# Optimization experiments

Hardware: AMD Instinct MI355X
Metric: run time of the kernel (lower is better)

The kernel has to match this reference:

```python
import jax, jax.numpy as jnp
import numpy as np

KNN_K = 16
EPS = 1e-5


def _knn_idx(p, k):
    # p: [B,3,N] -> idx [B,N,k] of nearest neighbors (self excluded)
    pt = jnp.swapaxes(p, 1, 2)                      # [B,N,3]
    xx = jnp.sum(pt * pt, axis=-1)                  # [B,N]
    inner = jnp.einsum('bnd,bmd->bnm', pt, pt)      # [B,N,N]
    dist = -(xx[:, :, None] - 2.0 * inner + xx[:, None, :])  # -||pi-pj||^2
    N = pt.shape[1]
    dist = dist - 1e9 * jnp.eye(N, dtype=dist.dtype)
    return jax.lax.top_k(dist, k)[1]


def _ln(x, g, b):
    mu = jnp.mean(x, axis=-1, keepdims=True)
    var = jnp.mean((x - mu) ** 2, axis=-1, keepdims=True)
    return (x - mu) * jax.lax.rsqrt(var + EPS) * g + b


_gather = jax.vmap(lambda a, i: a[i])  # a:[N,C], i:[N,k] -> [N,k,C]


def setup_inputs() -> dict:
    key = jax.random.key(0)
    ks = jax.random.split(key, 24)
    Cin, C, B, N = 64, 128, 8, 2048
    s = lambda k_, shp, fan: jax.random.normal(k_, shp, jnp.float32) * (1.0 / np.sqrt(fan))
    return {
        'x': jax.random.normal(ks[0], (B, Cin, N), jnp.float32),
        'p': jax.random.normal(ks[1], (B, 3, N), jnp.float32),
        'Win': s(ks[2], (C, Cin), Cin), 'bin_': jnp.zeros((C,), jnp.float32),
        'Wq': s(ks[3], (C, C), C), 'Wk': s(ks[4], (C, C), C), 'Wv': s(ks[5], (C, C), C),
        'Wd1': s(ks[6], (C, 3), 3), 'bd1': jnp.zeros((C,), jnp.float32),
        'Wd2': s(ks[7], (C, C), C), 'bd2': jnp.zeros((C,), jnp.float32),
        'Wa': s(ks[8], (C, C), C), 'ba': jnp.zeros((C,), jnp.float32),
        'g1': jnp.ones((C,), jnp.float32), 'b1': jnp.zeros((C,), jnp.float32),
        'g2': jnp.ones((C,), jnp.float32), 'b2': jnp.zeros((C,), jnp.float32),
        'Wf1': s(ks[9], (4 * C, C), C), 'bf1': jnp.zeros((4 * C,), jnp.float32),
        'Wf2': s(ks[10], (C, 4 * C), 4 * C), 'bf2': jnp.zeros((C,), jnp.float32),
    }


def reference(x, p, Win, bin_, Wq, Wk, Wv, Wd1, bd1, Wd2, bd2, Wa, ba,
              g1, b1, g2, b2, Wf1, bf1, Wf2, bf2) -> jnp.ndarray:
    B, _, N = x.shape
    k = min(KNN_K, max(1, N - 1))
    # in_proj (conv1x1 == per-point linear); work in [B,N,C]
    h = jnp.einsum('oc,bcn->bno', Win, x) + bin_          # [B,N,C]
    hn = _ln(h, g1, b1)
    idx = _knn_idx(p, k)                                  # [B,N,k] (int)
    q = hn @ Wq.T                                         # [B,N,C]
    k_all = hn @ Wk.T
    v_all = hn @ Wv.T
    k_j = _gather(k_all, idx)                             # [B,N,k,C]
    v_j = _gather(v_all, idx)
    pt = jnp.swapaxes(p, 1, 2)                            # [B,N,3]
    p_j = _gather(pt, idx)                                # [B,N,k,3]
    rel = pt[:, :, None, :] - p_j                         # [B,N,k,3]
    d = jax.nn.relu(rel @ Wd1.T + bd1) @ Wd2.T + bd2      # [B,N,k,C]
    logits = (q[:, :, None, :] - k_j + d) @ Wa.T + ba     # [B,N,k,C]
    a = jax.nn.softmax(logits, axis=2)                    # softmax over neighbors
    y = jnp.sum(a * (v_j + d), axis=2)                    # [B,N,C]
    h = h + y
    h2 = _ln(h, g2, b2)
    h = h + jax.nn.relu(h2 @ Wf1.T + bf1) @ Wf2.T + bf2
    return jnp.swapaxes(h, 1, 2)                          # [B,C,N]
```

## Files before the change

### kernel.cpp

```cpp
#include <hip/hip_runtime.h>

typedef __bf16 bf16_t;
typedef __bf16 bf16x8 __attribute__((ext_vector_type(8)));
typedef __bf16 bf16x2 __attribute__((ext_vector_type(2)));
typedef float  f32x4  __attribute__((ext_vector_type(4)));

#define MFMA16(a,b,c) __builtin_amdgcn_mfma_f32_16x16x32_bf16((a),(b),(c),0,0,0)

#define BB 8
#define NN 2048
#define CC 128
#define CIN 64
#define KNB 16
#define BNT (BB*NN)

static __device__ __forceinline__ int remap256(int x) { return ((x & 7) << 5) | (x >> 3); }

static __device__ __forceinline__ bf16x8 cvt8(const float* src) {
  f32x4 a0 = *(const f32x4*)src;
  f32x4 a1 = *(const f32x4*)(src + 4);
  bf16x8 fr;
  fr[0] = (__bf16)a0[0]; fr[1] = (__bf16)a0[1]; fr[2] = (__bf16)a0[2]; fr[3] = (__bf16)a0[3];
  fr[4] = (__bf16)a1[0]; fr[5] = (__bf16)a1[1]; fr[6] = (__bf16)a1[2]; fr[7] = (__bf16)a1[3];
  return fr;
}

__global__ __launch_bounds__(256) void compw_k(
    const float* __restrict__ Wq, const float* __restrict__ Wk, const float* __restrict__ Wv,
    const float* __restrict__ Wd2, const float* __restrict__ Wa,
    const float* __restrict__ Wf1, const float* __restrict__ Wf2,
    bf16_t* __restrict__ Wqb, bf16_t* __restrict__ Wkb, bf16_t* __restrict__ Wvb,
    bf16_t* __restrict__ Wd2b, bf16_t* __restrict__ Wab,
    bf16_t* __restrict__ Wf1b, bf16_t* __restrict__ Wf2b) {
  int mat = blockIdx.y;
  int nel = (mat >= 5) ? 65536 : 16384;
  const float* S = mat == 0 ? Wq : mat == 1 ? Wk : mat == 2 ? Wv : mat == 3 ? Wd2
                 : mat == 4 ? Wa : mat == 5 ? Wf1 : Wf2;
  bf16_t* D = mat == 0 ? Wqb : mat == 1 ? Wkb : mat == 2 ? Wvb : mat == 3 ? Wd2b
            : mat == 4 ? Wab : mat == 5 ? Wf1b : Wf2b;
  for (int i = blockIdx.x * 256 + threadIdx.x; i * 8 < nel; i += 2048)
    *(bf16x8*)(D + i * 8) = cvt8(S + i * 8);
}

__global__ __launch_bounds__(256) void inproj_ln_k(
    const float* __restrict__ x, const float* __restrict__ Win, const float* __restrict__ bin,
    const float* __restrict__ g1, const float* __restrict__ b1,
    float* __restrict__ h, bf16_t* __restrict__ hnb) {
  __shared__ bf16_t As[64 * 72];
  __shared__ bf16_t Bs[128 * 72];
  __shared__ float hs[64 * 132];
  int t = threadIdx.x;
  int lane = t & 63, w = t >> 6, quad = lane >> 4, l15 = lane & 15;
  int mBase = remap256(blockIdx.x) * 64;
  int b = mBase >> 11, n0 = mBase & (NN - 1);
  const float* xb = x + (size_t)b * CIN * NN;
  {
    int k = t >> 2, part = t & 3;
    #pragma unroll
    for (int i = 0; i < 4; ++i) {
      f32x4 v = *(const f32x4*)(xb + (size_t)k * NN + n0 + part * 16 + i * 4);
      #pragma unroll
      for (int j2 = 0; j2 < 4; ++j2) As[(part * 16 + i * 4 + j2) * 72 + k] = (__bf16)v[j2];
    }
  }
  {
    int row = t >> 1, seg = (t & 1) * 32;
    #pragma unroll
    for (int i = 0; i < 4; ++i)
      *(bf16x8*)(&Bs[row * 72 + seg + i * 8]) = cvt8(Win + (size_t)row * CIN + seg + i * 8);
  }
  __syncthreads();
  f32x4 acc[2][4] = {};
  #pragma unroll
  for (int s = 0; s < 2; ++s) {
    bf16x8 af[4];
    #pragma unroll
    for (int mt = 0; mt < 4; ++mt)
      af[mt] = *(const bf16x8*)(&As[(mt * 16 + l15) * 72 + s * 32 + quad * 8]);
    #pragma unroll
    for (int t2 = 0; t2 < 2; ++t2) {
      bf16x8 bfr = *(const bf16x8*)(&Bs[((w * 2 + t2) * 16 + l15) * 72 + s * 32 + quad * 8]);
      #pragma unroll
      for (int mt = 0; mt < 4; ++mt) acc[t2][mt] = MFMA16(af[mt], bfr, acc[t2][mt]);
    }
  }
  #pragma unroll
  for (int t2 = 0; t2 < 2; ++t2) {
    int col = (w * 2 + t2) * 16 + l15;
    float bv = bin[col];
    #pragma unroll
    for (int mt = 0; mt < 4; ++mt)
      #pragma unroll
      for (int reg = 0; reg < 4; ++reg)
        hs[(mt * 16 + quad * 4 + reg) * 132 + col] = acc[t2][mt][reg] + bv;
  }
  __syncthreads();
  {
    int row = t >> 2, c0 = (t & 3) * 32;
    float v[32];
    #pragma unroll
    for (int i = 0; i < 8; ++i) *(f32x4*)(v + i * 4) = *(const f32x4*)(&hs[row * 132 + c0 + i * 4]);
    float s1 = 0.f, s2 = 0.f;
    #pragma unroll
    for (int i = 0; i < 32; ++i) { s1 += v[i]; s2 += v[i] * v[i]; }
    s1 += __shfl_xor(s1, 1); s1 += __shfl_xor(s1, 2);
    s2 += __shfl_xor(s2, 1); s2 += __shfl_xor(s2, 2);
    float mu = s1 * (1.f / CC);
    float var = s2 * (1.f / CC) - mu * mu;
    float rs = rsqrtf(var + 1e-5f);
    float* hrow = h + (size_t)(mBase + row) * CC + c0;
    #pragma unroll
    for (int i = 0; i < 8; ++i) *(f32x4*)(hrow + i * 4) = *(const f32x4*)(v + i * 4);
    bf16_t* hnrow = hnb + (size_t)(mBase + row) * CC + c0;
    #pragma unroll
    for (int i = 0; i < 4; ++i) {
      f32x4 g4a = ((const f32x4*)g1)[(c0 >> 2) + i * 2],     g4b = ((const f32x4*)g1)[(c0 >> 2) + i * 2 + 1];
      f32x4 b4a = ((const f32x4*)b1)[(c0 >> 2) + i * 2],     b4b = ((const f32x4*)b1)[(c0 >> 2) + i * 2 + 1];
      bf16x8 o;
      #pragma unroll
      for (int j = 0; j < 4; ++j) o[j]     = (__bf16)((v[i * 8 + j]     - mu) * rs * g4a[j] + b4a[j]);
      #pragma unroll
      for (int j = 0; j < 4; ++j) o[4 + j] = (__bf16)((v[i * 8 + 4 + j] - mu) * rs * g4b[j] + b4b[j]);
      *(bf16x8*)(hnrow + i * 8) = o;
    }
  }
}

static __device__ __forceinline__ void cas(double& a, double& b) {
  double lo = fmin(a, b), hi = fmax(a, b); a = lo; b = hi;
}
#define S8(K,o) \
  cas(K[o+0],K[o+1]); cas(K[o+2],K[o+3]); cas(K[o+4],K[o+5]); cas(K[o+6],K[o+7]); \
  cas(K[o+0],K[o+2]); cas(K[o+1],K[o+3]); cas(K[o+4],K[o+6]); cas(K[o+5],K[o+7]); \
  cas(K[o+1],K[o+2]); cas(K[o+5],K[o+6]); \
  cas(K[o+0],K[o+4]); cas(K[o+1],K[o+5]); cas(K[o+2],K[o+6]); cas(K[o+3],K[o+7]); \
  cas(K[o+2],K[o+4]); cas(K[o+3],K[o+5]); \
  cas(K[o+1],K[o+2]); cas(K[o+3],K[o+4]); cas(K[o+5],K[o+6]);
#define M8(K,a,b) \
  K[a+0]=fmin(K[a+0],K[b+7]); K[a+1]=fmin(K[a+1],K[b+6]); K[a+2]=fmin(K[a+2],K[b+5]); K[a+3]=fmin(K[a+3],K[b+4]); \
  K[a+4]=fmin(K[a+4],K[b+3]); K[a+5]=fmin(K[a+5],K[b+2]); K[a+6]=fmin(K[a+6],K[b+1]); K[a+7]=fmin(K[a+7],K[b+0]); \
  cas(K[a+0],K[a+4]); cas(K[a+1],K[a+5]); cas(K[a+2],K[a+6]); cas(K[a+3],K[a+7]); \
  cas(K[a+0],K[a+2]); cas(K[a+1],K[a+3]); cas(K[a+4],K[a+6]); cas(K[a+5],K[a+7]); \
  cas(K[a+0],K[a+1]); cas(K[a+2],K[a+3]); cas(K[a+4],K[a+5]); cas(K[a+6],K[a+7]);

static __device__ void knn_impl(float* sp, const float* __restrict__ p,
                                int* __restrict__ idxo, int bid) {
  float* px = sp; float* py = sp + NN; float* pz = sp + 2 * NN;
  int t = threadIdx.x;
  int b = bid >> 9;
  int g = bid & 511;
  const float* pb = p + (size_t)b * 3 * NN;
  for (int i = t; i < NN; i += 256) { px[i] = pb[i]; py[i] = pb[NN + i]; pz[i] = pb[2 * NN + i]; }
  __syncthreads();
  int w = t >> 6, lane = t & 63;
  int n = g * 4 + w;
  float pnx = px[n], pny = py[n], pnz = pz[n];
  double key[32];
  #pragma unroll
  for (int s = 0; s < 32; ++s) {
    int m = s * 64 + lane;
    float dx = pnx - px[m], dy = pny - py[m], dz = pnz - pz[m];
    float dist = dx * dx + dy * dy + dz * dz;
    unsigned db = (m == n) ? 0x7F800000u : __float_as_uint(dist);
    key[s] = __hiloint2double((int)db, m);
  }
  S8(key, 0); S8(key, 8); S8(key, 16); S8(key, 24);
  M8(key, 0, 8); M8(key, 16, 24); M8(key, 0, 16);
  const double DINF = __hiloint2double(0x7F900000, 0);
  int* myout = idxo + ((size_t)b * NN + n) * KNB;
  #pragma unroll 1
  for (int r = 0; r < 16; ++r) {
    double gm = key[0];
    #pragma unroll
    for (int off = 1; off < 64; off <<= 1) {
      double o = __shfl_xor(gm, off);
      gm = fmin(gm, o);
    }
    if (lane == 0) myout[r] = __double2loint(gm);
    bool win = (key[0] == gm);
    key[0] = win ? key[1] : key[0];
    key[1] = win ? key[2] : key[1];
    key[2] = win ? key[3] : key[2];
    key[3] = win ? key[4] : key[3];
    key[4] = win ? key[5] : key[4];
    key[5] = win ? key[6] : key[5];
    key[6] = win ? key[7] : key[6];
    key[7] = win ? DINF   : key[7];
  }
}

template<int EPI>
static __device__ void gemm_body(bf16_t* As, bf16_t* Bs,
    const bf16_t* __restrict__ Ab, const bf16_t* __restrict__ Wb, const float* __restrict__ bias,
    float* __restrict__ outF, bf16_t* __restrict__ outB, const float* __restrict__ resid,
    int mBase, int nBase, int Ncol, int Kdim) {
  int t = threadIdx.x;
  int lane = t & 63, w = t >> 6, quad = lane >> 4, l15 = lane & 15;
  int r = t >> 2, seg = (t & 3) * 8;
  f32x4 acc[4] = {{0,0,0,0},{0,0,0,0},{0,0,0,0},{0,0,0,0}};
  for (int k0 = 0; k0 < Kdim; k0 += 32) {
    __syncthreads();
    *(bf16x8*)(&As[r * 40 + seg]) = *(const bf16x8*)(Ab + (size_t)(mBase + r) * Kdim + k0 + seg);
    *(bf16x8*)(&Bs[r * 40 + seg]) = *(const bf16x8*)(Wb + (size_t)(nBase + r) * Kdim + k0 + seg);
    __syncthreads();
    bf16x8 bfr = *(const bf16x8*)(&Bs[(w * 16 + l15) * 40 + quad * 8]);
    #pragma unroll
    for (int mt = 0; mt < 4; ++mt) {
      bf16x8 afr = *(const bf16x8*)(&As[(mt * 16 + l15) * 40 + quad * 8]);
      acc[mt] = MFMA16(afr, bfr, acc[mt]);
    }
  }
  int n = nBase + w * 16 + l15;
  float bv = bias ? bias[n] : 0.f;
  #pragma unroll
  for (int mt = 0; mt < 4; ++mt) {
    #pragma unroll
    for (int reg = 0; reg < 4; ++reg) {
      int m = mBase + mt * 16 + quad * 4 + reg;
      float val = acc[mt][reg] + bv;
      if (EPI == 0) {
        outF[(size_t)m * Ncol + n] = val;
      } else if (EPI == 1) {
        outB[(size_t)m * Ncol + n] = (__bf16)fmaxf(val, 0.f);
      } else if (EPI == 3) {
        outB[(size_t)m * Ncol + n] = (__bf16)val;
      } else {
        val += resid[(size_t)m * CC + n];
        int bo = m >> 11, np = m & (NN - 1);
        outF[((size_t)bo * CC + n) * NN + np] = val;
      }
    }
  }
}

template<int EPI>
__global__ __launch_bounds__(256) void gemm_k(
    const bf16_t* __restrict__ Ab, const bf16_t* __restrict__ Wb, const float* __restrict__ bias,
    float* __restrict__ outF, bf16_t* __restrict__ outB, const float* __restrict__ resid,
    int Ncol, int Kdim) {
  __shared__ bf16_t As[64 * 40];
  __shared__ bf16_t Bs[64 * 40];
  gemm_body<EPI>(As, Bs, Ab, Wb, bias, outF, outB, resid,
                 remap256(blockIdx.x) * 64, blockIdx.y * 64, Ncol, Kdim);
}

__global__ __launch_bounds__(256) void knn_qkv_k(
    const float* __restrict__ p, int* __restrict__ idxo,
    const bf16_t* __restrict__ hnb,
    const bf16_t* __restrict__ Wqb, const bf16_t* __restrict__ Wkb, const bf16_t* __restrict__ Wvb,
    float* __restrict__ q, bf16_t* __restrict__ kb, bf16_t* __restrict__ vb) {
  __shared__ __align__(16) char smem[3 * NN * 4];
  if (blockIdx.x < 4096) {
    knn_impl((float*)smem, p, idxo, blockIdx.x);
  } else {
    bf16_t* As = (bf16_t*)smem;
    bf16_t* Bs = As + 64 * 40;
    int bx = blockIdx.x - 4096;
    int yy = bx >> 8, xx = bx & 255;
    int sel = yy >> 1;
    int mB = remap256(xx) * 64, nB = (yy & 1) * 64;
    if (sel == 0)      gemm_body<0>(As, Bs, hnb, Wqb, nullptr, q,  nullptr, nullptr, mB, nB, CC, CC);
    else if (sel == 1) gemm_body<3>(As, Bs, hnb, Wkb, nullptr, nullptr, kb, nullptr, mB, nB, CC, CC);
    else               gemm_body<3>(As, Bs, hnb, Wvb, nullptr, nullptr, vb, nullptr, mB, nB, CC, CC);
  }
}

__global__ __launch_bounds__(256, 3) void attn_k(
    const float* __restrict__ qbuf, const bf16_t* __restrict__ kbuf, const bf16_t* __restrict__ vbuf,
    const float* __restrict__ p, const int* __restrict__ idx,
    const float* __restrict__ Wd1, const float* __restrict__ bd1,
    const bf16_t* __restrict__ Wd2b, const float* __restrict__ bd2,
    const bf16_t* __restrict__ Wab, const float* __restrict__ ba,
    const float* __restrict__ g2, const float* __restrict__ b2,
    const float* __restrict__ h, float* __restrict__ hres, bf16_t* __restrict__ h2) {
  __shared__ bf16_t ts[64 * 136];
  __shared__ float hrs[4 * 128];
  __shared__ f32x4 wd1s[128];
  __shared__ f32x4 rels4[64];
  __shared__ int idxs[64];
  int t = threadIdx.x;
  int lane = t & 63, w = t >> 6, quad = lane >> 4, l15 = lane & 15;
  int batch = blockIdx.x & 7, grp = blockIdx.x >> 3;
  int bn0 = batch * NN + grp * 4;
  int b = batch;
  const float* pb = p + (size_t)b * 3 * NN;
  int col0 = w * 32 + l15;
  int col1 = col0 + 16;

  bf16x8 Bd[2][4];
  #pragma unroll
  for (int t2 = 0; t2 < 2; ++t2) {
    int row = w * 32 + t2 * 16 + l15;
    #pragma unroll
    for (int s = 0; s < 4; ++s)
      Bd[t2][s] = *(const bf16x8*)(Wd2b + (size_t)row * CC + s * 32 + quad * 8);
  }

  if (t < 64) {
    int jj = idx[(size_t)bn0 * KNB + t];
    idxs[t] = jj;
    int npt = grp * 4 + (t >> 4);
    f32x4 rv;
    rv[0] = pb[npt]          - pb[jj];
    rv[1] = pb[NN + npt]     - pb[NN + jj];
    rv[2] = pb[2 * NN + npt] - pb[2 * NN + jj];
    rv[3] = 0.f;
    rels4[t] = rv;
  }
  if (t < 128) {
    f32x4 wv;
    wv[0] = Wd1[t * 3]; wv[1] = Wd1[t * 3 + 1]; wv[2] = Wd1[t * 3 + 2]; wv[3] = bd1[t];
    wd1s[t] = wv;
  }
  __syncthreads();

  float qv[2][4];
  #pragma unroll
  for (int mt = 0; mt < 4; ++mt) {
    qv[0][mt] = qbuf[(size_t)(bn0 + mt) * CC + col0];
    qv[1][mt] = qbuf[(size_t)(bn0 + mt) * CC + col1];
  }
  float kreg[2][4][4];
  #pragma unroll
  for (int mt = 0; mt < 4; ++mt)
    #pragma unroll
    for (int reg = 0; reg < 4; ++reg) {
      size_t base = (size_t)(b * NN + idxs[mt * 16 + quad * 4 + reg]) * CC;
      kreg[0][mt][reg] = (float)kbuf[base + col0];
      kreg[1][mt][reg] = (float)kbuf[base + col1];
    }

  f32x4 relv[4];
  #pragma unroll
  for (int mt = 0; mt < 4; ++mt) relv[mt] = rels4[mt * 16 + l15];
  f32x4 accd[2][4] = {};
  #pragma unroll
  for (int s = 0; s < 4; ++s) {
    bf16x8 af[4];
    #pragma unroll
    for (int j = 0; j < 8; ++j) {
      f32x4 wv = wd1s[s * 32 + quad * 8 + j];
      #pragma unroll
      for (int mt = 0; mt < 4; ++mt) {
        float tv = fmaf(wv[0], relv[mt][0], fmaf(wv[1], relv[mt][1], fmaf(wv[2], relv[mt][2], wv[3])));
        af[mt][j] = (__bf16)fmaxf(tv, 0.f);
      }
    }
    #pragma unroll
    for (int t2 = 0; t2 < 2; ++t2)
      #pragma unroll
      for (int mt = 0; mt < 4; ++mt)
        accd[t2][mt] = MFMA16(af[mt], Bd[t2][s], accd[t2][mt]);
  }

  {
    float b2v0 = bd2[col0], b2v1 = bd2[col1];
    #pragma unroll
    for (int mt = 0; mt < 4; ++mt)
      #pragma unroll
      for (int reg = 0; reg < 4; ++reg) {
        int row = mt * 16 + quad * 4 + reg;
        float d0 = accd[0][mt][reg] + b2v0;
        float d1 = accd[1][mt][reg] + b2v1;
        accd[0][mt][reg] = d0;
        accd[1][mt][reg] = d1;
        ts[row * 136 + col0] = (__bf16)(qv[0][mt] - kreg[0][mt][reg] + d0);
        ts[row * 136 + col1] = (__bf16)(qv[1][mt] - kreg[1][mt][reg] + d1);
      }
  }
  __syncthreads();

  float vreg[2][4][4];
  #pragma unroll
  for (int mt = 0; mt < 4; ++mt)
    #pragma unroll
    for (int reg = 0; reg < 4; ++reg) {
      size_t base = (size_t)(b * NN + idxs[mt * 16 + quad * 4 + reg]) * CC;
      vreg[0][mt][reg] = (float)vbuf[base + col0];
      vreg[1][mt][reg] = (float)vbuf[base + col1];
    }
  float hv[2][4];
  if (quad == 0) {
    #pragma unroll
    for (int mt = 0; mt < 4; ++mt) {
      hv[0][mt] = h[(size_t)(bn0 + mt) * CC + col0];
      hv[1][mt] = h[(size_t)(bn0 + mt) * CC + col1];
    }
  }
  bf16x8 Ba[2][4];
  #pragma unroll
  for (int t2 = 0; t2 < 2; ++t2) {
    int row = w * 32 + t2 * 16 + l15;
    #pragma unroll
    for (int s = 0; s < 4; ++s)
      Ba[t2][s] = *(const bf16x8*)(Wab + (size_t)row * CC + s * 32 + quad * 8);
  }

  f32x4 accl[2][4] = {};
  #pragma unroll
  for (int s = 0; s < 4; ++s) {
    bf16x8 af[4];
    #pragma unroll
    for (int mt = 0; mt < 4; ++mt)
      af[mt] = *(const bf16x8*)(&ts[(mt * 16 + l15) * 136 + s * 32 + quad * 8]);
    #pragma unroll
    for (int t2 = 0; t2 < 2; ++t2)
      #pragma unroll
      for (int mt = 0; mt < 4; ++mt)
        accl[t2][mt] = MFMA16(af[mt], Ba[t2][s], accl[t2][mt]);
  }

  #pragma unroll
  for (int t2 = 0; t2 < 2; ++t2) {
    int col = t2 ? col1 : col0;
    float bav = ba[col];
    #pragma unroll
    for (int mt = 0; mt < 4; ++mt) {
      float lv0 = accl[t2][mt][0] + bav, lv1 = accl[t2][mt][1] + bav;
      float lv2 = accl[t2][mt][2] + bav, lv3 = accl[t2][mt][3] + bav;
      float mx = fmaxf(fmaxf(lv0, lv1), fmaxf(lv2, lv3));
      mx = fmaxf(mx, __shfl_xor(mx, 16));
      mx = fmaxf(mx, __shfl_xor(mx, 32));
      float e0 = __expf(lv0 - mx), e1 = __expf(lv1 - mx);
      float e2 = __expf(lv2 - mx), e3 = __expf(lv3 - mx);
      float ss = e0 + e1 + e2 + e3;
      ss += __shfl_xor(ss, 16); ss += __shfl_xor(ss, 32);
      float yv = e0 * (vreg[t2][mt][0] + accd[t2][mt][0])
               + e1 * (vreg[t2][mt][1] + accd[t2][mt][1])
               + e2 * (vreg[t2][mt][2] + accd[t2][mt][2])
               + e3 * (vreg[t2][mt][3] + accd[t2][mt][3]);
      yv += __shfl_xor(yv, 16); yv += __shfl_xor(yv, 32);
      if (quad == 0) {
        float hvv = hv[t2][mt] + yv / ss;
        hres[(size_t)(bn0 + mt) * CC + col] = hvv;
        hrs[mt * 128 + col] = hvv;
      }
    }
  }
  __syncthreads();

  {
    int c0 = lane * 2;
    float v0 = hrs[w * 128 + c0], v1 = hrs[w * 128 + c0 + 1];
    float s1 = v0 + v1, s2 = v0 * v0 + v1 * v1;
    #pragma unroll
    for (int off = 1; off < 64; off <<= 1) { s1 += __shfl_xor(s1, off); s2 += __shfl_xor(s2, off); }
    float mu = s1 * (1.f / CC);
    float var = s2 * (1.f / CC) - mu * mu;
    float rs = rsqrtf(var + 1e-5f);
    bf16x2 o;
    o[0] = (__bf16)((v0 - mu) * rs * g2[c0] + b2[c0]);
    o[1] = (__bf16)((v1 - mu) * rs * g2[c0 + 1] + b2[c0 + 1]);
    *(bf16x2*)(h2 + (size_t)(bn0 + w) * CC + c0) = o;
  }
}

extern "C" void kernel_launch(void* const* d_in, const int* in_sizes, int n_in,
                              void* d_out, int out_size, void* d_ws, size_t ws_size,
                              hipStream_t stream) {
  const float* x   = (const float*)d_in[0];
  const float* p   = (const float*)d_in[1];
  const float* Win = (const float*)d_in[2];
  const float* bin = (const float*)d_in[3];
  const float* Wq  = (const float*)d_in[4];
  const float* Wk  = (const float*)d_in[5];
  const float* Wv  = (const float*)d_in[6];
  const float* Wd1 = (const float*)d_in[7];
  const float* bd1 = (const float*)d_in[8];
  const float* Wd2 = (const float*)d_in[9];
  const float* bd2 = (const float*)d_in[10];
  const float* Wa  = (const float*)d_in[11];
  const float* ba  = (const float*)d_in[12];
  const float* g1  = (const float*)d_in[13];
  const float* b1  = (const float*)d_in[14];
  const float* g2  = (const float*)d_in[15];
  const float* b2  = (const float*)d_in[16];
  const float* Wf1 = (const float*)d_in[17];
  const float* bf1 = (const float*)d_in[18];
  const float* Wf2 = (const float*)d_in[19];
  const float* bf2 = (const float*)d_in[20];
  float* out = (float*)d_out;

  const size_t SZ = (size_t)BNT * CC;
  float* wsf = (float*)d_ws;
  float*  h    = wsf;
  bf16_t* hnb  = (bf16_t*)(wsf + SZ);
  float*  hres = wsf + SZ;
  float*  q    = wsf + 2 * SZ;
  bf16_t* kb   = (bf16_t*)(wsf + 3 * SZ);
  bf16_t* vb   = kb + SZ;
  bf16_t* g    = (bf16_t*)(wsf + 2 * SZ);
  bf16_t* h2   = (bf16_t*)(wsf + 4 * SZ);
  int*    idxw = (int*)(wsf + 4 * SZ + SZ / 2);
  bf16_t* Wqb  = (bf16_t*)(idxw + (size_t)BNT * KNB);
  bf16_t* Wkb  = Wqb  + 16384;
  bf16_t* Wvb  = Wkb  + 16384;
  bf16_t* Wd2b = Wvb  + 16384;
  bf16_t* Wab  = Wd2b + 16384;
  bf16_t* Wf1b = Wab  + 16384;
  bf16_t* Wf2b = Wf1b + 65536;

  compw_k<<<dim3(8, 7), 256, 0, stream>>>(Wq, Wk, Wv, Wd2, Wa, Wf1, Wf2,
                                          Wqb, Wkb, Wvb, Wd2b, Wab, Wf1b, Wf2b);
  inproj_ln_k<<<BNT / 64, 256, 0, stream>>>(x, Win, bin, g1, b1, h, hnb);
  knn_qkv_k<<<4096 + 1536, 256, 0, stream>>>(p, idxw, hnb, Wqb, Wkb, Wvb, q, kb, vb);
  attn_k<<<BNT / 4, 256, 0, stream>>>(q, kb, vb, p, idxw, Wd1, bd1, Wd2b, bd2, Wab, ba,
                                      g2, b2, h, hres, h2);
  gemm_k<1><<<dim3(BNT / 64, 8), 256, 0, stream>>>(h2, Wf1b, bf1, nullptr, g, nullptr, 4 * CC, CC);
  gemm_k<2><<<dim3(BNT / 64, 2), 256, 0, stream>>>(g, Wf2b, bf2, out, nullptr, hres, CC, 4 * CC);
}
```

Measured before the change: 266.0 us.

## Store h, q and residual in bf16 and fuse weight conversion into in-projection

```diff
diff --git a/kernel.cpp b/kernel.cpp
--- a/kernel.cpp
+++ b/kernel.cpp
@@ -25,31 +25,32 @@
   return fr;
 }
 
-__global__ __launch_bounds__(256) void compw_k(
+__global__ __launch_bounds__(256) void inproj_compw_k(
+    const float* __restrict__ x, const float* __restrict__ Win, const float* __restrict__ bin,
+    const float* __restrict__ g1, const float* __restrict__ b1,
+    bf16_t* __restrict__ hb, bf16_t* __restrict__ hnb,
     const float* __restrict__ Wq, const float* __restrict__ Wk, const float* __restrict__ Wv,
     const float* __restrict__ Wd2, const float* __restrict__ Wa,
     const float* __restrict__ Wf1, const float* __restrict__ Wf2,
     bf16_t* __restrict__ Wqb, bf16_t* __restrict__ Wkb, bf16_t* __restrict__ Wvb,
     bf16_t* __restrict__ Wd2b, bf16_t* __restrict__ Wab,
     bf16_t* __restrict__ Wf1b, bf16_t* __restrict__ Wf2b) {
-  int mat = blockIdx.y;
-  int nel = (mat >= 5) ? 65536 : 16384;
-  const float* S = mat == 0 ? Wq : mat == 1 ? Wk : mat == 2 ? Wv : mat == 3 ? Wd2
-                 : mat == 4 ? Wa : mat == 5 ? Wf1 : Wf2;
-  bf16_t* D = mat == 0 ? Wqb : mat == 1 ? Wkb : mat == 2 ? Wvb : mat == 3 ? Wd2b
-            : mat == 4 ? Wab : mat == 5 ? Wf1b : Wf2b;
-  for (int i = blockIdx.x * 256 + threadIdx.x; i * 8 < nel; i += 2048)
-    *(bf16x8*)(D + i * 8) = cvt8(S + i * 8);
-}
-
-__global__ __launch_bounds__(256) void inproj_ln_k(
-    const float* __restrict__ x, const float* __restrict__ Win, const float* __restrict__ bin,
-    const float* __restrict__ g1, const float* __restrict__ b1,
-    float* __restrict__ h, bf16_t* __restrict__ hnb) {
   __shared__ bf16_t As[64 * 72];
   __shared__ bf16_t Bs[128 * 72];
   __shared__ float hs[64 * 132];
   int t = threadIdx.x;
+  if (blockIdx.x >= 256) {
+    int bi = blockIdx.x - 256;
+    int mat = bi >> 3, xi = bi & 7;
+    int nel = (mat >= 5) ? 65536 : 16384;
+    const float* S = mat == 0 ? Wq : mat == 1 ? Wk : mat == 2 ? Wv : mat == 3 ? Wd2
+                   : mat == 4 ? Wa : mat == 5 ? Wf1 : Wf2;
+    bf16_t* D = mat == 0 ? Wqb : mat == 1 ? Wkb : mat == 2 ? Wvb : mat == 3 ? Wd2b
+              : mat == 4 ? Wab : mat == 5 ? Wf1b : Wf2b;
+    for (int i = xi * 256 + t; i * 8 < nel; i += 2048)
+      *(bf16x8*)(D + i * 8) = cvt8(S + i * 8);
+    return;
+  }
   int lane = t & 63, w = t >> 6, quad = lane >> 4, l15 = lane & 15;
   int mBase = remap256(blockIdx.x) * 64;
   int b = mBase >> 11, n0 = mBase & (NN - 1);
@@ -108,9 +109,14 @@
     float mu = s1 * (1.f / CC);
     float var = s2 * (1.f / CC) - mu * mu;
     float rs = rsqrtf(var + 1e-5f);
-    float* hrow = h + (size_t)(mBase + row) * CC + c0;
-    #pragma unroll
-    for (int i = 0; i < 8; ++i) *(f32x4*)(hrow + i * 4) = *(const f32x4*)(v + i * 4);
+    bf16_t* hrow = hb + (size_t)(mBase + row) * CC + c0;
+    #pragma unroll
+    for (int i = 0; i < 4; ++i) {
+      bf16x8 ho;
+      #pragma unroll
+      for (int j = 0; j < 8; ++j) ho[j] = (__bf16)v[i * 8 + j];
+      *(bf16x8*)(hrow + i * 8) = ho;
+    }
     bf16_t* hnrow = hnb + (size_t)(mBase + row) * CC + c0;
     #pragma unroll
     for (int i = 0; i < 4; ++i) {
@@ -192,7 +198,7 @@
 template<int EPI>
 static __device__ void gemm_body(bf16_t* As, bf16_t* Bs,
     const bf16_t* __restrict__ Ab, const bf16_t* __restrict__ Wb, const float* __restrict__ bias,
-    float* __restrict__ outF, bf16_t* __restrict__ outB, const float* __restrict__ resid,
+    float* __restrict__ outF, bf16_t* __restrict__ outB, const bf16_t* __restrict__ resid,
     int mBase, int nBase, int Ncol, int Kdim) {
   int t = threadIdx.x;
   int lane = t & 63, w = t >> 6, quad = lane >> 4, l15 = lane & 15;
@@ -218,14 +224,12 @@
     for (int reg = 0; reg < 4; ++reg) {
       int m = mBase + mt * 16 + quad * 4 + reg;
       float val = acc[mt][reg] + bv;
-      if (EPI == 0) {
-        outF[(size_t)m * Ncol + n] = val;
-      } else if (EPI == 1) {
+      if (EPI == 1) {
         outB[(size_t)m * Ncol + n] = (__bf16)fmaxf(val, 0.f);
       } else if (EPI == 3) {
         outB[(size_t)m * Ncol + n] = (__bf16)val;
       } else {
-        val += resid[(size_t)m * CC + n];
+        val += (float)resid[(size_t)m * CC + n];
         int bo = m >> 11, np = m & (NN - 1);
         outF[((size_t)bo * CC + n) * NN + np] = val;
       }
@@ -236,7 +240,7 @@
 template<int EPI>
 __global__ __launch_bounds__(256) void gemm_k(
     const bf16_t* __restrict__ Ab, const bf16_t* __restrict__ Wb, const float* __restrict__ bias,
-    float* __restrict__ outF, bf16_t* __restrict__ outB, const float* __restrict__ resid,
+    float* __restrict__ outF, bf16_t* __restrict__ outB, const bf16_t* __restrict__ resid,
     int Ncol, int Kdim) {
   __shared__ bf16_t As[64 * 40];
   __shared__ bf16_t Bs[64 * 40];
@@ -248,7 +252,7 @@
     const float* __restrict__ p, int* __restrict__ idxo,
     const bf16_t* __restrict__ hnb,
     const bf16_t* __restrict__ Wqb, const bf16_t* __restrict__ Wkb, const bf16_t* __restrict__ Wvb,
-    float* __restrict__ q, bf16_t* __restrict__ kb, bf16_t* __restrict__ vb) {
+    bf16_t* __restrict__ qb, bf16_t* __restrict__ kb, bf16_t* __restrict__ vb) {
   __shared__ __align__(16) char smem[3 * NN * 4];
   if (blockIdx.x < 4096) {
     knn_impl((float*)smem, p, idxo, blockIdx.x);
@@ -259,20 +263,20 @@
     int yy = bx >> 8, xx = bx & 255;
     int sel = yy >> 1;
     int mB = remap256(xx) * 64, nB = (yy & 1) * 64;
-    if (sel == 0)      gemm_body<0>(As, Bs, hnb, Wqb, nullptr, q,  nullptr, nullptr, mB, nB, CC, CC);
+    if (sel == 0)      gemm_body<3>(As, Bs, hnb, Wqb, nullptr, nullptr, qb, nullptr, mB, nB, CC, CC);
     else if (sel == 1) gemm_body<3>(As, Bs, hnb, Wkb, nullptr, nullptr, kb, nullptr, mB, nB, CC, CC);
     else               gemm_body<3>(As, Bs, hnb, Wvb, nullptr, nullptr, vb, nullptr, mB, nB, CC, CC);
   }
 }
 
-__global__ __launch_bounds__(256, 3) void attn_k(
-    const float* __restrict__ qbuf, const bf16_t* __restrict__ kbuf, const bf16_t* __restrict__ vbuf,
+__global__ __launch_bounds__(256, 4) void attn_k(
+    const bf16_t* __restrict__ qbuf, const bf16_t* __restrict__ kbuf, const bf16_t* __restrict__ vbuf,
     const float* __restrict__ p, const int* __restrict__ idx,
     const float* __restrict__ Wd1, const float* __restrict__ bd1,
     const bf16_t* __restrict__ Wd2b, const float* __restrict__ bd2,
     const bf16_t* __restrict__ Wab, const float* __restrict__ ba,
     const float* __restrict__ g2, const float* __restrict__ b2,
-    const float* __restrict__ h, float* __restrict__ hres, bf16_t* __restrict__ h2) {
+    const bf16_t* __restrict__ hb, bf16_t* __restrict__ hresb, bf16_t* __restrict__ h2) {
   __shared__ bf16_t ts[64 * 136];
   __shared__ float hrs[4 * 128];
   __shared__ f32x4 wd1s[128];
@@ -317,8 +321,8 @@
   float qv[2][4];
   #pragma unroll
   for (int mt = 0; mt < 4; ++mt) {
-    qv[0][mt] = qbuf[(size_t)(bn0 + mt) * CC + col0];
-    qv[1][mt] = qbuf[(size_t)(bn0 + mt) * CC + col1];
+    qv[0][mt] = (float)qbuf[(size_t)(bn0 + mt) * CC + col0];
+    qv[1][mt] = (float)qbuf[(size_t)(bn0 + mt) * CC + col1];
   }
   float kreg[2][4][4];
   #pragma unroll
@@ -383,8 +387,8 @@
   if (quad == 0) {
     #pragma unroll
     for (int mt = 0; mt < 4; ++mt) {
-      hv[0][mt] = h[(size_t)(bn0 + mt) * CC + col0];
-      hv[1][mt] = h[(size_t)(bn0 + mt) * CC + col1];
+      hv[0][mt] = (float)hb[(size_t)(bn0 + mt) * CC + col0];
+      hv[1][mt] = (float)hb[(size_t)(bn0 + mt) * CC + col1];
     }
   }
   bf16x8 Ba[2][4];
@@ -432,7 +436,7 @@
       yv += __shfl_xor(yv, 16); yv += __shfl_xor(yv, 32);
       if (quad == 0) {
         float hvv = hv[t2][mt] + yv / ss;
-        hres[(size_t)(bn0 + mt) * CC + col] = hvv;
+        hresb[(size_t)(bn0 + mt) * CC + col] = (__bf16)hvv;
         hrs[mt * 128 + col] = hvv;
       }
     }
@@ -483,29 +487,29 @@
 
   const size_t SZ = (size_t)BNT * CC;
   float* wsf = (float*)d_ws;
-  float*  h    = wsf;
-  bf16_t* hnb  = (bf16_t*)(wsf + SZ);
-  float*  hres = wsf + SZ;
-  float*  q    = wsf + 2 * SZ;
-  bf16_t* kb   = (bf16_t*)(wsf + 3 * SZ);
-  bf16_t* vb   = kb + SZ;
-  bf16_t* g    = (bf16_t*)(wsf + 2 * SZ);
-  bf16_t* h2   = (bf16_t*)(wsf + 4 * SZ);
-  int*    idxw = (int*)(wsf + 4 * SZ + SZ / 2);
-  bf16_t* Wqb  = (bf16_t*)(idxw + (size_t)BNT * KNB);
-  bf16_t* Wkb  = Wqb  + 16384;
-  bf16_t* Wvb  = Wkb  + 16384;
-  bf16_t* Wd2b = Wvb  + 16384;
-  bf16_t* Wab  = Wd2b + 16384;
-  bf16_t* Wf1b = Wab  + 16384;
-  bf16_t* Wf2b = Wf1b + 65536;
-
-  compw_k<<<dim3(8, 7), 256, 0, stream>>>(Wq, Wk, Wv, Wd2, Wa, Wf1, Wf2,
-                                          Wqb, Wkb, Wvb, Wd2b, Wab, Wf1b, Wf2b);
-  inproj_ln_k<<<BNT / 64, 256, 0, stream>>>(x, Win, bin, g1, b1, h, hnb);
-  knn_qkv_k<<<4096 + 1536, 256, 0, stream>>>(p, idxw, hnb, Wqb, Wkb, Wvb, q, kb, vb);
-  attn_k<<<BNT / 4, 256, 0, stream>>>(q, kb, vb, p, idxw, Wd1, bd1, Wd2b, bd2, Wab, ba,
-                                      g2, b2, h, hres, h2);
+  bf16_t* hb    = (bf16_t*)wsf;
+  bf16_t* hnb   = (bf16_t*)(wsf + SZ / 2);
+  bf16_t* hresb = hnb;
+  bf16_t* qb    = (bf16_t*)(wsf + SZ);
+  bf16_t* kb    = (bf16_t*)(wsf + SZ + SZ / 2);
+  bf16_t* vb    = (bf16_t*)(wsf + 2 * SZ);
+  bf16_t* g     = (bf16_t*)(wsf + SZ);
+  bf16_t* h2    = (bf16_t*)(wsf + 3 * SZ);
+  int*    idxw  = (int*)(wsf + 3 * SZ + SZ / 2);
+  bf16_t* Wqb   = (bf16_t*)(idxw + (size_t)BNT * KNB);
+  bf16_t* Wkb   = Wqb  + 16384;
+  bf16_t* Wvb   = Wkb  + 16384;
+  bf16_t* Wd2b  = Wvb  + 16384;
+  bf16_t* Wab   = Wd2b + 16384;
+  bf16_t* Wf1b  = Wab  + 16384;
+  bf16_t* Wf2b  = Wf1b + 65536;
+
+  inproj_compw_k<<<256 + 56, 256, 0, stream>>>(x, Win, bin, g1, b1, hb, hnb,
+                                               Wq, Wk, Wv, Wd2, Wa, Wf1, Wf2,
+                                               Wqb, Wkb, Wvb, Wd2b, Wab, Wf1b, Wf2b);
+  knn_qkv_k<<<4096 + 1536, 256, 0, stream>>>(p, idxw, hnb, Wqb, Wkb, Wvb, qb, kb, vb);
+  attn_k<<<BNT / 4, 256, 0, stream>>>(qb, kb, vb, p, idxw, Wd1, bd1, Wd2b, bd2, Wab, ba,
+                                      g2, b2, hb, hresb, h2);
   gemm_k<1><<<dim3(BNT / 64, 8), 256, 0, stream>>>(h2, Wf1b, bf1, nullptr, g, nullptr, 4 * CC, CC);
-  gemm_k<2><<<dim3(BNT / 64, 2), 256, 0, stream>>>(g, Wf2b, bf2, out, nullptr, hres, CC, 4 * CC);
-}
+  gemm_k<2><<<dim3(BNT / 64, 2), 256, 0, stream>>>(g, Wf2b, bf2, out, nullptr, hresb, CC, 4 * CC);
+}
```

Result: slower. 308.2 us (+15.9%).
